# Kernel tuning notes

Hardware: AMD Instinct MI355X
Metric: run time of the kernel (lower is better)

Reference implementation:

```python
import jax, jax.numpy as jnp
import numpy as np

N = 40000      # num nodes
E = 640000     # num edges (avg degree 16)
D = 128        # hidden_size
L = 2          # num_gcn


def setup_inputs() -> dict:
    key = jax.random.key(0)
    k1, k2, k3, k4, k5, k6 = jax.random.split(key, 6)
    h = jax.random.normal(k1, (N, D), dtype=jnp.float32)
    edge_src = jax.random.randint(k2, (E,), 0, N, dtype=jnp.int32)
    edge_dst = jax.random.randint(k3, (E,), 0, N, dtype=jnp.int32)
    w_self = jax.random.uniform(k4, (E,), dtype=jnp.float32)
    w_ppi = jax.random.uniform(k5, (E,), dtype=jnp.float32)
    # Xavier-uniform linear weights, zero bias (matches reset_parameters)
    limit = float(np.sqrt(6.0 / (D + D)))
    W = jax.random.uniform(k6, (L, D, D), dtype=jnp.float32, minval=-limit, maxval=limit)
    b = jnp.zeros((L, D), dtype=jnp.float32)
    return {"h": h, "edge_src": edge_src, "edge_dst": edge_dst,
            "w_self": w_self, "w_ppi": w_ppi, "W": W, "b": b}


def _agg(h, src, dst, w):
    # edge-weighted SpMM: sum over incoming edges of w_e * h[src_e]
    msgs = h[src] * w[:, None]                       # [E, D]
    return jax.ops.segment_sum(msgs, dst, num_segments=N)  # [N, D]


def reference(h, edge_src, edge_dst, w_self, w_ppi, W, b):
    for l in range(L):
        res = _agg(h, edge_src, edge_dst, w_self)        # residual aggregation
        ppi = _agg(h, edge_src, edge_dst, w_ppi)         # ppi aggregation
        # NodeUpdate: dropout(relu(linear(ppi))) + res  (dropout=0 -> identity)
        h = jax.nn.relu(ppi @ W[l].T + b[l]) + res
    return h
```

## Files before the change

### kernel.cpp

```cpp
#include <hip/hip_runtime.h>

#define D 128
#define TILE 16
#define CAP 64

typedef short bf16x8 __attribute__((ext_vector_type(8)));
typedef float f32x4  __attribute__((ext_vector_type(4)));
typedef float f32x2  __attribute__((ext_vector_type(2)));

static __device__ __forceinline__ unsigned f2bf(float x) {
    unsigned u = __float_as_uint(x);
    return (u + 0x7FFFu + ((u >> 16) & 1u)) >> 16;
}
static __device__ __forceinline__ float blo(unsigned v) { return __uint_as_float(v << 16); }
static __device__ __forceinline__ float bhi(unsigned v) { return __uint_as_float(v & 0xFFFF0000u); }

__global__ __launch_bounds__(256) void cvt2z_kernel(const float4* __restrict__ a,
                                                    uint2* __restrict__ oa, int n4a,
                                                    const float4* __restrict__ bsrc,
                                                    uint2* __restrict__ ob, int n4b,
                                                    int4* __restrict__ zbuf, int nz4) {
    int i = blockIdx.x * 256 + threadIdx.x;
    if (i < n4a) {
        float4 v = a[i];
        uint2 o;
        o.x = f2bf(v.x) | (f2bf(v.y) << 16);
        o.y = f2bf(v.z) | (f2bf(v.w) << 16);
        oa[i] = o;
    }
    int j = i - n4a;
    if (j >= 0 && j < n4b) {
        float4 v = bsrc[j];
        uint2 o;
        o.x = f2bf(v.x) | (f2bf(v.y) << 16);
        o.y = f2bf(v.z) | (f2bf(v.w) << 16);
        ob[j] = o;
    }
    int k = j - n4b;
    if (k >= 0 && k < nz4) zbuf[k] = make_int4(0, 0, 0, 0);
}

__global__ __launch_bounds__(256) void build_kernel(const int* __restrict__ src,
                                                    const int* __restrict__ dst,
                                                    const float* __restrict__ wself,
                                                    const float* __restrict__ wppi,
                                                    int* __restrict__ cnt,
                                                    uint2* __restrict__ edges, int E) {
    int i = blockIdx.x * 256 + threadIdx.x;
    if (i < E) {
        int d = dst[i];
        int r = atomicAdd(&cnt[d], 1);
        if (r < CAP) {
            uint2 e;
            e.x = (unsigned)src[i];
            e.y = f2bf(wself[i]) | (f2bf(wppi[i]) << 16);
            edges[(d << 6) + r] = e;
        }
    }
}

static __device__ __forceinline__ void edge_fma(uint2 er, uint4 hv, float sc,
                                                f32x2 (&ra)[4], f32x2 (&pa)[4]) {
    float a = blo(er.y) * sc, b = bhi(er.y) * sc;
    f32x2 av = {a, a}, bv = {b, b};
    f32x2 h01 = {blo(hv.x), bhi(hv.x)};
    f32x2 h23 = {blo(hv.y), bhi(hv.y)};
    f32x2 h45 = {blo(hv.z), bhi(hv.z)};
    f32x2 h67 = {blo(hv.w), bhi(hv.w)};
    ra[0] = __builtin_elementwise_fma(av, h01, ra[0]);
    ra[1] = __builtin_elementwise_fma(av, h23, ra[1]);
    ra[2] = __builtin_elementwise_fma(av, h45, ra[2]);
    ra[3] = __builtin_elementwise_fma(av, h67, ra[3]);
    pa[0] = __builtin_elementwise_fma(bv, h01, pa[0]);
    pa[1] = __builtin_elementwise_fma(bv, h23, pa[1]);
    pa[2] = __builtin_elementwise_fma(bv, h45, pa[2]);
    pa[3] = __builtin_elementwise_fma(bv, h67, pa[3]);
}

static __device__ __forceinline__ void agg_node(const unsigned short* __restrict__ h16,
                                                const uint2* __restrict__ edges,
                                                const uint2 (&er)[8], int cn, int beg,
                                                int q, int c8, int nn,
                                                f32x2 (&ra)[4], f32x2 (&pa)[4]) {
    unsigned s[8]; float sc[8];
    #pragma unroll
    for (int j = 0; j < 8; ++j) {
        int slot = 4 * j + q;
        bool act = slot < cn;
        unsigned sj = act ? er[j].x : er[0].x;
        s[j] = sj < (unsigned)nn ? sj : 0u;
        sc[j] = act ? 1.f : 0.f;
    }
    uint4 hv[8];
    #pragma unroll
    for (int j = 0; j < 4; ++j)
        hv[j] = *(const uint4*)(h16 + (size_t)s[j] * D + c8 * 8);
    if (cn > 16) {
        #pragma unroll
        for (int j = 4; j < 8; ++j)
            hv[j] = *(const uint4*)(h16 + (size_t)s[j] * D + c8 * 8);
    }
    #pragma unroll
    for (int j = 0; j < 4; ++j) edge_fma(er[j], hv[j], sc[j], ra, pa);
    if (cn > 16) {
        #pragma unroll
        for (int j = 4; j < 8; ++j) edge_fma(er[j], hv[j], sc[j], ra, pa);
    }
    if (cn > 32) {
        int end = beg + cn;
        for (int e = beg + 32; e < end; e += 16) {
            uint2 err[4]; float scc[4];
            #pragma unroll
            for (int j = 0; j < 4; ++j) {
                int idx = e + 4 * j + q;
                bool act = idx < end;
                err[j] = edges[act ? idx : beg];
                scc[j] = act ? 1.f : 0.f;
            }
            uint4 hh[4];
            #pragma unroll
            for (int j = 0; j < 4; ++j) {
                unsigned sj = err[j].x < (unsigned)nn ? err[j].x : 0u;
                hh[j] = *(const uint4*)(h16 + (size_t)sj * D + c8 * 8);
            }
            #pragma unroll
            for (int j = 0; j < 4; ++j) edge_fma(err[j], hh[j], scc[j], ra, pa);
        }
    }
}

__global__ __launch_bounds__(512, 4) void layer_kernel(const unsigned short* __restrict__ h16,
                                                       const int* __restrict__ cnt,
                                                       const uint2* __restrict__ edges,
                                                       const unsigned short* __restrict__ Wb,
                                                       const float* __restrict__ bias,
                                                       float* __restrict__ out,
                                                       unsigned short* __restrict__ out16,
                                                       int n) {
    __shared__ unsigned short ppi_lds[TILE][136];
    __shared__ float          res_lds[TILE][132];
    int t = threadIdx.x;
    int w = t >> 6, lane = t & 63;
    int tile = blockIdx.x;
    int q  = lane >> 4;
    int c8 = lane & 15;

    int m16 = lane & 15, quad = lane >> 4;
    bf16x8 bfr[4];
    const unsigned short* brow = Wb + (size_t)(w * 16 + m16) * D + quad * 8;
    #pragma unroll
    for (int kt = 0; kt < 4; ++kt) bfr[kt] = *(const bf16x8*)(brow + kt * 32);
    float bb = bias[w * 16 + m16];

    int cn[2], beg[2];
    uint2 er[2][8];
    #pragma unroll
    for (int sub = 0; sub < 2; ++sub) {
        int node = tile * TILE + sub * 8 + w;
        beg[sub] = node << 6;
        cn[sub]  = cnt[node];
        #pragma unroll
        for (int j = 0; j < 8; ++j) er[sub][j] = edges[beg[sub] + 4 * j + q];
    }

    #pragma unroll
    for (int sub = 0; sub < 2; ++sub) {
        int nd = sub * 8 + w;
        int c = cn[sub] < CAP ? cn[sub] : CAP;
        f32x2 ra[4] = {{0.f,0.f},{0.f,0.f},{0.f,0.f},{0.f,0.f}};
        f32x2 pa[4] = {{0.f,0.f},{0.f,0.f},{0.f,0.f},{0.f,0.f}};
        if (c > 0)
            agg_node(h16, edges, er[sub], c, beg[sub], q, c8, n, ra, pa);

        float r[8] = {ra[0].x, ra[0].y, ra[1].x, ra[1].y, ra[2].x, ra[2].y, ra[3].x, ra[3].y};
        float p[8] = {pa[0].x, pa[0].y, pa[1].x, pa[1].y, pa[2].x, pa[2].y, pa[3].x, pa[3].y};
        #pragma unroll
        for (int i = 0; i < 8; ++i) {
            r[i] += __shfl_xor(r[i], 16, 64);
            r[i] += __shfl_xor(r[i], 32, 64);
            p[i] += __shfl_xor(p[i], 16, 64);
            p[i] += __shfl_xor(p[i], 32, 64);
        }
        if (q == 0) {
            *(float4*)&res_lds[nd][c8 * 8]     = make_float4(r[0], r[1], r[2], r[3]);
            *(float4*)&res_lds[nd][c8 * 8 + 4] = make_float4(r[4], r[5], r[6], r[7]);
            uint4 o;
            o.x = f2bf(p[0]) | (f2bf(p[1]) << 16);
            o.y = f2bf(p[2]) | (f2bf(p[3]) << 16);
            o.z = f2bf(p[4]) | (f2bf(p[5]) << 16);
            o.w = f2bf(p[6]) | (f2bf(p[7]) << 16);
            *(uint4*)&ppi_lds[nd][c8 * 8] = o;
        }
    }
    __syncthreads();

    {
        bf16x8 a[4];
        const unsigned short* arow = &ppi_lds[m16][quad * 8];
        #pragma unroll
        for (int kt = 0; kt < 4; ++kt) a[kt] = *(const bf16x8*)(arow + kt * 32);

        f32x4 acc = {0.f, 0.f, 0.f, 0.f};
        #pragma unroll
        for (int kt = 0; kt < 4; ++kt)
            acc = __builtin_amdgcn_mfma_f32_16x16x32_bf16(a[kt], bfr[kt], acc, 0, 0, 0);

        int o = w * 16 + m16;
        #pragma unroll
        for (int r = 0; r < 4; ++r) {
            int nd = quad * 4 + r;
            float v = fmaxf(acc[r] + bb, 0.f) + res_lds[nd][o];
            size_t gi = (size_t)(tile * TILE + nd) * D + o;
            if (out)   out[gi] = v;
            if (out16) out16[gi] = (unsigned short)f2bf(v);
        }
    }
}

extern "C" void kernel_launch(void* const* d_in, const int* in_sizes, int n_in,
                              void* d_out, int out_size, void* d_ws, size_t ws_size,
                              hipStream_t stream) {
    const float* h0    = (const float*)d_in[0];
    const int*   esrc  = (const int*)d_in[1];
    const int*   edst  = (const int*)d_in[2];
    const float* wself = (const float*)d_in[3];
    const float* wppi  = (const float*)d_in[4];
    const float* W     = (const float*)d_in[5];
    const float* b     = (const float*)d_in[6];
    float*       out   = (float*)d_out;

    const int N = in_sizes[0] / D;
    const int E = in_sizes[1];
    const int L = in_sizes[5] / (D * D);

    char* ws = (char*)d_ws;
    unsigned short* h16a  = (unsigned short*)ws; ws += (size_t)N * D * 2;
    unsigned short* h16b  = (unsigned short*)ws; ws += (size_t)N * D * 2;
    uint2*          edges = (uint2*)ws;          ws += (size_t)N * CAP * 8;
    unsigned short* Wb    = (unsigned short*)ws; ws += (size_t)L * D * D * 2;
    int* cnt = (int*)ws;  ws += (size_t)N * 4;

    int n4h = N * D / 4;
    int n4w = L * D * D / 4;
    int nz4 = N / 4;
    int tot = n4h + n4w + nz4;
    cvt2z_kernel<<<(tot + 255) / 256, 256, 0, stream>>>(
        (const float4*)h0, (uint2*)h16a, n4h,
        (const float4*)W, (uint2*)Wb, n4w,
        (int4*)cnt, nz4);

    int eb = (E + 255) / 256;
    build_kernel<<<eb, 256, 0, stream>>>(esrc, edst, wself, wppi, cnt, edges, E);

    int ntiles = N / TILE;
    layer_kernel<<<ntiles, 512, 0, stream>>>(h16a, cnt, edges, Wb, b,
                                             (L > 1) ? nullptr : out,
                                             (L > 1) ? h16b : nullptr, N);
    for (int l = 1; l < L; ++l) {
        bool last = (l + 1 == L);
        layer_kernel<<<ntiles, 512, 0, stream>>>(h16b, cnt, edges,
                                                 Wb + (size_t)l * D * D, b + (size_t)l * D,
                                                 last ? out : nullptr,
                                                 last ? nullptr : h16a, N);
        unsigned short* tmp = h16a; h16a = h16b; h16b = tmp;
    }
}
```

Before: 193.1 us.

## Switch storage and aggregation from bf16/fp32 to packed fp16 arithmetic

Stores features, weights and edge weights as fp16 instead of bf16, and accumulates the edge-weighted aggregation with packed fp16 FMAs instead of fp32 pairs. The cross-lane reductions also run on packed fp16 pairs, which halves the shuffle count, and the matmul uses the fp16 MFMA. This cuts conversion ALU work and register pressure in the gather loop. The cost is lower accumulation precision and a risk of fp16 overflow or rounding error, since sums over up to 64 edges now accumulate in half precision.

Result: faster. 182.5 us (-5.5%).

```diff
diff --git a/kernel.cpp b/kernel.cpp
--- a/kernel.cpp
+++ b/kernel.cpp
@@ -4,16 +4,14 @@
 #define TILE 16
 #define CAP 64
 
-typedef short bf16x8 __attribute__((ext_vector_type(8)));
+typedef _Float16 f16x2 __attribute__((ext_vector_type(2)));
+typedef _Float16 f16x8 __attribute__((ext_vector_type(8)));
 typedef float f32x4  __attribute__((ext_vector_type(4)));
-typedef float f32x2  __attribute__((ext_vector_type(2)));
-
-static __device__ __forceinline__ unsigned f2bf(float x) {
-    unsigned u = __float_as_uint(x);
-    return (u + 0x7FFFu + ((u >> 16) & 1u)) >> 16;
-}
-static __device__ __forceinline__ float blo(unsigned v) { return __uint_as_float(v << 16); }
-static __device__ __forceinline__ float bhi(unsigned v) { return __uint_as_float(v & 0xFFFF0000u); }
+
+static __device__ __forceinline__ unsigned pk2h(float a, float b) {
+    auto h = __builtin_amdgcn_cvt_pkrtz(a, b);
+    return __builtin_bit_cast(unsigned, h);
+}
 
 __global__ __launch_bounds__(256) void cvt2z_kernel(const float4* __restrict__ a,
                                                     uint2* __restrict__ oa, int n4a,
@@ -24,16 +22,16 @@
     if (i < n4a) {
         float4 v = a[i];
         uint2 o;
-        o.x = f2bf(v.x) | (f2bf(v.y) << 16);
-        o.y = f2bf(v.z) | (f2bf(v.w) << 16);
+        o.x = pk2h(v.x, v.y);
+        o.y = pk2h(v.z, v.w);
         oa[i] = o;
     }
     int j = i - n4a;
     if (j >= 0 && j < n4b) {
         float4 v = bsrc[j];
         uint2 o;
-        o.x = f2bf(v.x) | (f2bf(v.y) << 16);
-        o.y = f2bf(v.z) | (f2bf(v.w) << 16);
+        o.x = pk2h(v.x, v.y);
+        o.y = pk2h(v.z, v.w);
         ob[j] = o;
     }
     int k = j - n4b;
@@ -53,43 +51,44 @@
         if (r < CAP) {
             uint2 e;
             e.x = (unsigned)src[i];
-            e.y = f2bf(wself[i]) | (f2bf(wppi[i]) << 16);
+            e.y = pk2h(wself[i], wppi[i]);
             edges[(d << 6) + r] = e;
         }
     }
 }
 
-static __device__ __forceinline__ void edge_fma(uint2 er, uint4 hv, float sc,
-                                                f32x2 (&ra)[4], f32x2 (&pa)[4]) {
-    float a = blo(er.y) * sc, b = bhi(er.y) * sc;
-    f32x2 av = {a, a}, bv = {b, b};
-    f32x2 h01 = {blo(hv.x), bhi(hv.x)};
-    f32x2 h23 = {blo(hv.y), bhi(hv.y)};
-    f32x2 h45 = {blo(hv.z), bhi(hv.z)};
-    f32x2 h67 = {blo(hv.w), bhi(hv.w)};
-    ra[0] = __builtin_elementwise_fma(av, h01, ra[0]);
-    ra[1] = __builtin_elementwise_fma(av, h23, ra[1]);
-    ra[2] = __builtin_elementwise_fma(av, h45, ra[2]);
-    ra[3] = __builtin_elementwise_fma(av, h67, ra[3]);
-    pa[0] = __builtin_elementwise_fma(bv, h01, pa[0]);
-    pa[1] = __builtin_elementwise_fma(bv, h23, pa[1]);
-    pa[2] = __builtin_elementwise_fma(bv, h45, pa[2]);
-    pa[3] = __builtin_elementwise_fma(bv, h67, pa[3]);
+static __device__ __forceinline__ void edge_fma(unsigned wbits, uint4 hv,
+                                                f16x2 (&ra)[4], f16x2 (&pa)[4]) {
+    f16x2 wv = __builtin_bit_cast(f16x2, wbits);
+    f16x2 wa = {wv.x, wv.x};
+    f16x2 wb = {wv.y, wv.y};
+    f16x2 h01 = __builtin_bit_cast(f16x2, hv.x);
+    f16x2 h23 = __builtin_bit_cast(f16x2, hv.y);
+    f16x2 h45 = __builtin_bit_cast(f16x2, hv.z);
+    f16x2 h67 = __builtin_bit_cast(f16x2, hv.w);
+    ra[0] = __builtin_elementwise_fma(wa, h01, ra[0]);
+    ra[1] = __builtin_elementwise_fma(wa, h23, ra[1]);
+    ra[2] = __builtin_elementwise_fma(wa, h45, ra[2]);
+    ra[3] = __builtin_elementwise_fma(wa, h67, ra[3]);
+    pa[0] = __builtin_elementwise_fma(wb, h01, pa[0]);
+    pa[1] = __builtin_elementwise_fma(wb, h23, pa[1]);
+    pa[2] = __builtin_elementwise_fma(wb, h45, pa[2]);
+    pa[3] = __builtin_elementwise_fma(wb, h67, pa[3]);
 }
 
 static __device__ __forceinline__ void agg_node(const unsigned short* __restrict__ h16,
                                                 const uint2* __restrict__ edges,
                                                 const uint2 (&er)[8], int cn, int beg,
                                                 int q, int c8, int nn,
-                                                f32x2 (&ra)[4], f32x2 (&pa)[4]) {
-    unsigned s[8]; float sc[8];
+                                                f16x2 (&ra)[4], f16x2 (&pa)[4]) {
+    unsigned s[8], wz[8];
     #pragma unroll
     for (int j = 0; j < 8; ++j) {
         int slot = 4 * j + q;
         bool act = slot < cn;
         unsigned sj = act ? er[j].x : er[0].x;
-        s[j] = sj < (unsigned)nn ? sj : 0u;
-        sc[j] = act ? 1.f : 0.f;
+        s[j]  = sj < (unsigned)nn ? sj : 0u;
+        wz[j] = act ? er[j].y : 0u;
     }
     uint4 hv[8];
     #pragma unroll
@@ -101,21 +100,21 @@
             hv[j] = *(const uint4*)(h16 + (size_t)s[j] * D + c8 * 8);
     }
     #pragma unroll
-    for (int j = 0; j < 4; ++j) edge_fma(er[j], hv[j], sc[j], ra, pa);
+    for (int j = 0; j < 4; ++j) edge_fma(wz[j], hv[j], ra, pa);
     if (cn > 16) {
         #pragma unroll
-        for (int j = 4; j < 8; ++j) edge_fma(er[j], hv[j], sc[j], ra, pa);
+        for (int j = 4; j < 8; ++j) edge_fma(wz[j], hv[j], ra, pa);
     }
     if (cn > 32) {
         int end = beg + cn;
         for (int e = beg + 32; e < end; e += 16) {
-            uint2 err[4]; float scc[4];
+            uint2 err[4]; unsigned wzz[4];
             #pragma unroll
             for (int j = 0; j < 4; ++j) {
                 int idx = e + 4 * j + q;
                 bool act = idx < end;
                 err[j] = edges[act ? idx : beg];
-                scc[j] = act ? 1.f : 0.f;
+                wzz[j] = act ? err[j].y : 0u;
             }
             uint4 hh[4];
             #pragma unroll
@@ -124,9 +123,18 @@
                 hh[j] = *(const uint4*)(h16 + (size_t)sj * D + c8 * 8);
             }
             #pragma unroll
-            for (int j = 0; j < 4; ++j) edge_fma(err[j], hh[j], scc[j], ra, pa);
-        }
-    }
+            for (int j = 0; j < 4; ++j) edge_fma(wzz[j], hh[j], ra, pa);
+        }
+    }
+}
+
+static __device__ __forceinline__ unsigned red2(unsigned x) {
+    f16x2 a = __builtin_bit_cast(f16x2, x);
+    unsigned u = (unsigned)__shfl_xor((int)x, 16, 64);
+    a = a + __builtin_bit_cast(f16x2, u);
+    unsigned u2 = (unsigned)__shfl_xor((int)__builtin_bit_cast(unsigned, a), 32, 64);
+    a = a + __builtin_bit_cast(f16x2, u2);
+    return __builtin_bit_cast(unsigned, a);
 }
 
 __global__ __launch_bounds__(512, 4) void layer_kernel(const unsigned short* __restrict__ h16,
@@ -146,10 +154,10 @@
     int c8 = lane & 15;
 
     int m16 = lane & 15, quad = lane >> 4;
-    bf16x8 bfr[4];
-    const unsigned short* brow = Wb + (size_t)(w * 16 + m16) * D + quad * 8;
-    #pragma unroll
-    for (int kt = 0; kt < 4; ++kt) bfr[kt] = *(const bf16x8*)(brow + kt * 32);
+    f16x8 bfr[4];
+    const _Float16* brow = (const _Float16*)Wb + (size_t)(w * 16 + m16) * D + quad * 8;
+    #pragma unroll
+    for (int kt = 0; kt < 4; ++kt) bfr[kt] = *(const f16x8*)(brow + kt * 32);
     float bb = bias[w * 16 + m16];
 
     int cn[2], beg[2];
@@ -167,43 +175,42 @@
     for (int sub = 0; sub < 2; ++sub) {
         int nd = sub * 8 + w;
         int c = cn[sub] < CAP ? cn[sub] : CAP;
-        f32x2 ra[4] = {{0.f,0.f},{0.f,0.f},{0.f,0.f},{0.f,0.f}};
-        f32x2 pa[4] = {{0.f,0.f},{0.f,0.f},{0.f,0.f},{0.f,0.f}};
+        f16x2 ra[4] = {};
+        f16x2 pa[4] = {};
         if (c > 0)
             agg_node(h16, edges, er[sub], c, beg[sub], q, c8, n, ra, pa);
 
-        float r[8] = {ra[0].x, ra[0].y, ra[1].x, ra[1].y, ra[2].x, ra[2].y, ra[3].x, ra[3].y};
-        float p[8] = {pa[0].x, pa[0].y, pa[1].x, pa[1].y, pa[2].x, pa[2].y, pa[3].x, pa[3].y};
-        #pragma unroll
-        for (int i = 0; i < 8; ++i) {
-            r[i] += __shfl_xor(r[i], 16, 64);
-            r[i] += __shfl_xor(r[i], 32, 64);
-            p[i] += __shfl_xor(p[i], 16, 64);
-            p[i] += __shfl_xor(p[i], 32, 64);
-        }
+        unsigned v[8];
+        #pragma unroll
+        for (int i = 0; i < 4; ++i) v[i]     = red2(__builtin_bit_cast(unsigned, ra[i]));
+        #pragma unroll
+        for (int i = 0; i < 4; ++i) v[i + 4] = red2(__builtin_bit_cast(unsigned, pa[i]));
+
         if (q == 0) {
-            *(float4*)&res_lds[nd][c8 * 8]     = make_float4(r[0], r[1], r[2], r[3]);
-            *(float4*)&res_lds[nd][c8 * 8 + 4] = make_float4(r[4], r[5], r[6], r[7]);
-            uint4 o;
-            o.x = f2bf(p[0]) | (f2bf(p[1]) << 16);
-            o.y = f2bf(p[2]) | (f2bf(p[3]) << 16);
-            o.z = f2bf(p[4]) | (f2bf(p[5]) << 16);
-            o.w = f2bf(p[6]) | (f2bf(p[7]) << 16);
+            f16x2 r01 = __builtin_bit_cast(f16x2, v[0]);
+            f16x2 r23 = __builtin_bit_cast(f16x2, v[1]);
+            f16x2 r45 = __builtin_bit_cast(f16x2, v[2]);
+            f16x2 r67 = __builtin_bit_cast(f16x2, v[3]);
+            *(float4*)&res_lds[nd][c8 * 8]     = make_float4((float)r01.x, (float)r01.y,
+                                                             (float)r23.x, (float)r23.y);
+            *(float4*)&res_lds[nd][c8 * 8 + 4] = make_float4((float)r45.x, (float)r45.y,
+                                                             (float)r67.x, (float)r67.y);
+            uint4 o = make_uint4(v[4], v[5], v[6], v[7]);
             *(uint4*)&ppi_lds[nd][c8 * 8] = o;
         }
     }
     __syncthreads();
 
     {
-        bf16x8 a[4];
-        const unsigned short* arow = &ppi_lds[m16][quad * 8];
-        #pragma unroll
-        for (int kt = 0; kt < 4; ++kt) a[kt] = *(const bf16x8*)(arow + kt * 32);
+        f16x8 a[4];
+        const _Float16* arow = (const _Float16*)&ppi_lds[m16][quad * 8];
+        #pragma unroll
+        for (int kt = 0; kt < 4; ++kt) a[kt] = *(const f16x8*)(arow + kt * 32);
 
         f32x4 acc = {0.f, 0.f, 0.f, 0.f};
         #pragma unroll
         for (int kt = 0; kt < 4; ++kt)
-            acc = __builtin_amdgcn_mfma_f32_16x16x32_bf16(a[kt], bfr[kt], acc, 0, 0, 0);
+            acc = __builtin_amdgcn_mfma_f32_16x16x32_f16(a[kt], bfr[kt], acc, 0, 0, 0);
 
         int o = w * 16 + m16;
         #pragma unroll
@@ -212,7 +219,10 @@
             float v = fmaxf(acc[r] + bb, 0.f) + res_lds[nd][o];
             size_t gi = (size_t)(tile * TILE + nd) * D + o;
             if (out)   out[gi] = v;
-            if (out16) out16[gi] = (unsigned short)f2bf(v);
+            if (out16) {
+                _Float16 hvv = (_Float16)v;
+                out16[gi] = __builtin_bit_cast(unsigned short, hvv);
+            }
         }
     }
 }
```
